# Kernel tuning notes

Measured on AMD Instinct MI355X. Metric: run time of the kernel, lower is better.

Reference implementation:

```python
import jax, jax.numpy as jnp
import numpy as np
import math

A, R, E, H = 4, 2, 12, 24  # msg_angular, msg_radial, embed_dim, hidden_dim
N = A * R
B, L = 131072, 15

def _ring_adj(n):
    adj = np.zeros((n, n), np.float32)
    if n == 1:
        adj[0, 0] = 1.0
    else:
        for i in range(n):
            adj[i, (i - 1) % n] = 1.0
            adj[i, (i + 1) % n] = 1.0
    return jnp.asarray(adj)

ANG_ADJ = _ring_adj(A)
RAD_ADJ = _ring_adj(R)

def setup_inputs():
    key = jax.random.key(0)
    ks = jax.random.split(key, 16)
    p = lambda k, s: jax.random.normal(k, s, jnp.float32) * 0.1
    return {
        "x": jax.random.normal(ks[0], (B, L, 4), jnp.float32),
        "enc_w1": p(ks[1], (4, H)), "enc_b1": p(ks[2], (H,)),
        "enc_w2": p(ks[3], (H, H)), "enc_b2": p(ks[4], (H,)),
        "enc_w3": p(ks[5], (H, 3)), "enc_b3": p(ks[6], (3,)),
        "node_w1": p(ks[7], (E, H)), "node_b1": p(ks[8], (H,)),
        "node_w2": p(ks[9], (H, E)), "node_b2": p(ks[10], (E,)),
        "angular_logit": jnp.zeros((A,), jnp.float32),
        "radial_logit": jnp.zeros((R,), jnp.float32),
        "read_w1": p(ks[11], (E * N, H)), "read_b1": p(ks[12], (H,)),
        "read_w2": p(ks[13], (H, 4)), "read_b2": p(ks[14], (4,)),
    }

def _norm_adj(logit, adj):
    a = jax.nn.softmax(logit)[None, :] * adj
    return a / jnp.maximum(a.sum(1, keepdims=True), 1e-6)

def _forward(x, enc_w1, enc_b1, enc_w2, enc_b2, enc_w3, enc_b3,
             node_w1, node_b1, node_w2, node_b2,
             angular_logit, radial_logit,
             read_w1, read_b1, read_w2, read_b2):
    b = x.shape[0]
    # encoder: original loops over all timesteps but only uses the last z
    zt = jnp.tanh(x[:, -1, :] @ enc_w1 + enc_b1)
    zt = jnp.tanh(zt @ enc_w2 + enc_b2)
    z = zt @ enc_w3 + enc_b3                       # [B, 3]
    r = jax.nn.sigmoid(z[:, 0]) * (R - 1)          # R_idx in [0, R-1]
    p = (z[:, 1] + math.pi) / (2 * math.pi) * A    # phi_idx (can be <0 or >A)
    # torch code calls .item(), detaching indices/weights from autograd
    r = jax.lax.stop_gradient(r)
    p = jax.lax.stop_gradient(p)
    r0 = jnp.trunc(r)   # int() truncates toward zero
    p0 = jnp.trunc(p)
    dr = (r - r0)[:, None]
    dp = (p - p0)[:, None]
    dro = jnp.array([0.0, 0.0, 1.0, 1.0], jnp.float32)   # 4 bilinear corners
    dpo = jnp.array([0.0, 1.0, 0.0, 1.0], jnp.float32)
    wr = jnp.where(dro == 0, 1.0 - dr, dr)               # [B, 4]
    wp = jnp.where(dpo == 0, 1.0 - dp, dp)
    w = wr * wp                                          # [B, 4]
    r_i = jnp.minimum(r0.astype(jnp.int32)[:, None] + dro.astype(jnp.int32), R - 1)
    p_i = jnp.mod(p0.astype(jnp.int32)[:, None] + dpo.astype(jnp.int32), A)
    mask = (w > 0).astype(x.dtype)[:, :, None]           # 'if weight > 0' skip
    # node_embed = pad(concat([z, weight]), E); z entries are NOT weight-scaled
    vec = jnp.concatenate([
        jnp.broadcast_to(z[:, None, :], (b, 4, 3)),
        w[:, :, None],
        jnp.zeros((b, 4, E - 4), x.dtype)], axis=-1) * mask   # [B, 4, E]
    grid = jnp.zeros((b, R, A, E), x.dtype).at[
        jnp.arange(b)[:, None], r_i, p_i].add(vec)            # scatter-add
    h = grid.reshape(b, N, E)
    ang = _norm_adj(angular_logit, ANG_ADJ)  # [A, A]
    rad = _norm_adj(radial_logit, RAD_ADJ)   # [R, R]
    # faithful to the torch .view() layout mixing (r,a,e)
    h_ang = jnp.einsum('ij,bjk->bik', ang, h.reshape(b, A, R * E)).reshape(b, N, E)
    h_rad = jnp.einsum('ij,bjk->bik', rad, h.reshape(b, R, A * E)).reshape(b, N, E)
    h = h + h_ang + h_rad
    h = jnp.tanh(h @ node_w1 + node_b1) @ node_w2 + node_b2   # node_net
    out = jnp.tanh(h.reshape(b, -1) @ read_w1 + read_b1) @ read_w2 + read_b2
    return out  # [B, 4]

def reference(x, enc_w1, enc_b1, enc_w2, enc_b2, enc_w3, enc_b3,
              node_w1, node_b1, node_w2, node_b2,
              angular_logit, radial_logit,
              read_w1, read_b1, read_w2, read_b2):
    return _forward(x, enc_w1, enc_b1, enc_w2, enc_b2, enc_w3, enc_b3,
                    node_w1, node_b1, node_w2, node_b2,
                    angular_logit, radial_logit,
                    read_w1, read_b1, read_w2, read_b2)
```

## Files before the change

### kernel.cpp

```cpp
#include <hip/hip_runtime.h>
#include <math.h>


#define PI_F 3.14159265358979323846f

__device__ __forceinline__ float fast_tanh(float v) {
    float e = __expf(2.0f * v);
    return 1.0f - 2.0f * __builtin_amdgcn_rcpf(e + 1.0f);
}

__device__ __forceinline__ float quad_sum(float x) {
    x += __int_as_float(__builtin_amdgcn_update_dpp(
             0, __float_as_int(x), 0xB1, 0xF, 0xF, true));
    x += __int_as_float(__builtin_amdgcn_update_dpp(
             0, __float_as_int(x), 0x4E, 0xF, 0xF, true));
    return x;
}

#define K1_LDS 800

extern "C" __global__ void __launch_bounds__(256, 2)
topo_k1(const float* __restrict__ x,
        const float* __restrict__ ew1, const float* __restrict__ eb1,
        const float* __restrict__ ew2, const float* __restrict__ eb2,
        const float* __restrict__ ew3, const float* __restrict__ eb3,
        const float* __restrict__ alog, const float* __restrict__ rlog,
        float* __restrict__ ws, int B)
{
    __shared__ float wf[K1_LDS];
    const float4* wq = reinterpret_cast<const float4*>(wf);
    {
        const int tt = threadIdx.x;
        for (int i = tt; i < 96;  i += 256) wf[i]       = ew1[i];
        for (int i = tt; i < 24;  i += 256) wf[96 + i]  = eb1[i];
        for (int i = tt; i < 576; i += 256) wf[120 + i] = ew2[i];
        for (int i = tt; i < 24;  i += 256) wf[696 + i] = eb2[i];
        for (int i = tt; i < 72;  i += 256) wf[720 + (i % 3) * 24 + (i / 3)] = ew3[i];
        for (int i = tt; i < 3;   i += 256) wf[792 + i] = eb3[i];
    }
    __syncthreads();

    const int b = blockIdx.x * blockDim.x + threadIdx.x;
    if (b >= B) return;

    float ang[4][4];
    {
        float m = fmaxf(fmaxf(alog[0], alog[1]), fmaxf(alog[2], alog[3]));
        float e0 = __expf(alog[0] - m), e1 = __expf(alog[1] - m);
        float e2 = __expf(alog[2] - m), e3 = __expf(alog[3] - m);
        float s = e0 + e1 + e2 + e3;
        float sm[4] = { e0 / s, e1 / s, e2 / s, e3 / s };
        #pragma unroll
        for (int i = 0; i < 4; ++i) {
            const int jn = (i + 3) & 3, jp = (i + 1) & 3;
            float inv = 1.0f / fmaxf(sm[jn] + sm[jp], 1e-6f);
            #pragma unroll
            for (int j = 0; j < 4; ++j) {
                float adj = (j == jn || j == jp) ? 1.0f : 0.0f;
                ang[i][j] = sm[j] * adj * inv;
            }
        }
    }
    float rad[2][2];
    {
        float m = fmaxf(rlog[0], rlog[1]);
        float f0 = __expf(rlog[0] - m), f1 = __expf(rlog[1] - m);
        float fs = f0 + f1;
        float sm0 = f0 / fs, sm1 = f1 / fs;
        rad[0][0] = 0.0f; rad[0][1] = sm1 / fmaxf(sm1, 1e-6f);
        rad[1][1] = 0.0f; rad[1][0] = sm0 / fmaxf(sm0, 1e-6f);
    }

    const float4 xv = *reinterpret_cast<const float4*>(x + (size_t)b * 60 + 56);

    float zt[24];
    #pragma unroll
    for (int c = 0; c < 6; ++c) {
        float4 b4 = wq[24 + c];
        float4 w0 = wq[c],      w1 = wq[6 + c];
        float4 w2 = wq[12 + c], w3 = wq[18 + c];
        zt[c*4+0] = fast_tanh(b4.x + xv.x*w0.x + xv.y*w1.x + xv.z*w2.x + xv.w*w3.x);
        zt[c*4+1] = fast_tanh(b4.y + xv.x*w0.y + xv.y*w1.y + xv.z*w2.y + xv.w*w3.y);
        zt[c*4+2] = fast_tanh(b4.z + xv.x*w0.z + xv.y*w1.z + xv.z*w2.z + xv.w*w3.z);
        zt[c*4+3] = fast_tanh(b4.w + xv.x*w0.w + xv.y*w1.w + xv.z*w2.w + xv.w*w3.w);
    }

    float a2[24];
    #pragma unroll
    for (int c = 0; c < 6; ++c) {
        float4 b4 = wq[174 + c];
        a2[c*4+0] = b4.x; a2[c*4+1] = b4.y; a2[c*4+2] = b4.z; a2[c*4+3] = b4.w;
    }
    #pragma unroll
    for (int k = 0; k < 24; ++k) {
        const float zk = zt[k];
        #pragma unroll
        for (int c = 0; c < 6; ++c) {
            float4 wv = wq[30 + k * 6 + c];
            a2[c*4+0] += zk * wv.x; a2[c*4+1] += zk * wv.y;
            a2[c*4+2] += zk * wv.z; a2[c*4+3] += zk * wv.w;
        }
    }
    float zt2[24];
    #pragma unroll
    for (int j = 0; j < 24; ++j) zt2[j] = fast_tanh(a2[j]);

    float z0 = wf[792], z1 = wf[793], z2 = wf[794];
    #pragma unroll
    for (int c = 0; c < 6; ++c) {
        float4 v0 = wq[180 + c], v1 = wq[186 + c], v2 = wq[192 + c];
        z0 += zt2[c*4+0]*v0.x + zt2[c*4+1]*v0.y + zt2[c*4+2]*v0.z + zt2[c*4+3]*v0.w;
        z1 += zt2[c*4+0]*v1.x + zt2[c*4+1]*v1.y + zt2[c*4+2]*v1.z + zt2[c*4+3]*v1.w;
        z2 += zt2[c*4+0]*v2.x + zt2[c*4+1]*v2.y + zt2[c*4+2]*v2.z + zt2[c*4+3]*v2.w;
    }

    const float r = 1.0f / (1.0f + __expf(-z0));
    const float p = (z1 + PI_F) / (2.0f * PI_F) * 4.0f;
    const float r0f = truncf(r), p0f = truncf(p);
    const float dr = r - r0f, dp = p - p0f;
    const int r0i = (int)r0f, p0i = (int)p0f;

    const float w0c = (1.0f - dr) * (1.0f - dp);
    const float w1c = (1.0f - dr) * dp;
    const float w2c = dr * (1.0f - dp);
    const float w3c = dr * dp;

    const int ri0 = min(r0i, 1);
    const int ri2 = min(r0i + 1, 1);
    const int pi0 = p0i & 3;
    const int pi1 = (p0i + 1) & 3;

    const int c0 = ri0 * 4 + pi0, c1 = ri0 * 4 + pi1;
    const int c2 = ri2 * 4 + pi0, c3 = ri2 * 4 + pi1;

    float cnt[8], wsum[8];
    #pragma unroll
    for (int n = 0; n < 8; ++n) {
        float cm = 0.0f, cw = 0.0f;
        if (c0 == n && w0c > 0.0f) { cm += 1.0f; cw += w0c; }
        if (c1 == n && w1c > 0.0f) { cm += 1.0f; cw += w1c; }
        if (c2 == n && w2c > 0.0f) { cm += 1.0f; cw += w2c; }
        if (c3 == n && w3c > 0.0f) { cm += 1.0f; cw += w3c; }
        cnt[n] = cm; wsum[n] = cw;
    }
    float mc[8], mw[8];
    #pragma unroll
    for (int n = 0; n < 8; ++n) {
        float ac = cnt[n], aw = wsum[n];
        #pragma unroll
        for (int j = 0; j < 4; ++j) {
            const float g = ang[n >> 1][j];
            ac += g * cnt[2 * j + (n & 1)];
            aw += g * wsum[2 * j + (n & 1)];
        }
        #pragma unroll
        for (int j = 0; j < 2; ++j) {
            const float g = rad[n >> 2][j];
            ac += g * cnt[4 * j + (n & 3)];
            aw += g * wsum[4 * j + (n & 3)];
        }
        mc[n] = ac; mw[n] = aw;
    }

    float* wp = ws + (size_t)b * 20;
    float4 v0; v0.x = z0;    v0.y = z1;    v0.z = z2;    v0.w = 0.0f;
    float4 v1; v1.x = mc[0]; v1.y = mc[1]; v1.z = mc[2]; v1.w = mc[3];
    float4 v2; v2.x = mc[4]; v2.y = mc[5]; v2.z = mc[6]; v2.w = mc[7];
    float4 v3; v3.x = mw[0]; v3.y = mw[1]; v3.z = mw[2]; v3.w = mw[3];
    float4 v4; v4.x = mw[4]; v4.y = mw[5]; v4.z = mw[6]; v4.w = mw[7];
    reinterpret_cast<float4*>(wp)[0] = v0;
    reinterpret_cast<float4*>(wp)[1] = v1;
    reinterpret_cast<float4*>(wp)[2] = v2;
    reinterpret_cast<float4*>(wp)[3] = v3;
    reinterpret_cast<float4*>(wp)[4] = v4;
}

#define K2_LDS 2912

extern "C" __global__ void __launch_bounds__(256, 6)
topo_k2(const float* __restrict__ ws,
        const float* __restrict__ nw1, const float* __restrict__ nb1,
        const float* __restrict__ nw2, const float* __restrict__ nb2,
        const float* __restrict__ rw1, const float* __restrict__ rb1,
        const float* __restrict__ rw2, const float* __restrict__ rb2,
        float* __restrict__ out, int B)
{
    __shared__ float wf[K2_LDS];
    const float4* wq = reinterpret_cast<const float4*>(wf);

    {
        const int tt = threadIdx.x;
        for (int i = tt; i < 96;   i += 256) wf[i]        = nw1[i];
        for (int i = tt; i < 24;   i += 256) wf[96 + i]   = nb1[i];
        for (int i = tt; i < 288;  i += 256) wf[120 + i]  = nw2[i];
        for (int i = tt; i < 12;   i += 256) wf[408 + i]  = nb2[i];
        for (int i = tt; i < 2304; i += 256) {
            const int cell = i / 288, rem = i - cell * 288;
            wf[420 + cell * 296 + rem] = rw1[i];
        }
        for (int i = tt; i < 24;   i += 256) wf[2788 + i] = rb1[i];
        for (int i = tt; i < 96;   i += 256) wf[2812 + i] = rw2[i];
        for (int i = tt; i < 4;    i += 256) wf[2908 + i] = rb2[i];
    }
    __syncthreads();

    const int tid  = blockIdx.x * blockDim.x + threadIdx.x;
    const int lane = tid & 3;
    const int b    = tid >> 2;
    if (b >= B) return;

    const float* wp = ws + (size_t)b * 20;
    const float4 zv = *reinterpret_cast<const float4*>(wp);
    const float2 mc2 = *reinterpret_cast<const float2*>(wp + 4 + 2 * lane);
    const float2 mw2 = *reinterpret_cast<const float2*>(wp + 12 + 2 * lane);
    const float z0 = zv.x, z1 = zv.y, z2 = zv.z;

    float t[24];
    #pragma unroll
    for (int j = 0; j < 24; ++j) t[j] = 0.0f;

    #pragma unroll
    for (int cc = 0; cc < 2; ++cc) {
        const float mc_ = cc ? mc2.y : mc2.x;
        const float mw_ = cc ? mw2.y : mw2.x;
        const float f0 = mc_ * z0, f1 = mc_ * z1, f2 = mc_ * z2;

        float ho[12];
        {
            float4 bA = wq[102], bB = wq[103], bC = wq[104];
            ho[0] = bA.x; ho[1]  = bA.y; ho[2]  = bA.z; ho[3]  = bA.w;
            ho[4] = bB.x; ho[5]  = bB.y; ho[6]  = bB.z; ho[7]  = bB.w;
            ho[8] = bC.x; ho[9]  = bC.y; ho[10] = bC.z; ho[11] = bC.w;
        }
        #pragma unroll
        for (int c = 0; c < 6; ++c) {
            float4 b1 = wq[24 + c];
            float4 u0 = wq[c],      u1 = wq[6 + c];
            float4 u2 = wq[12 + c], u3 = wq[18 + c];
            float h[4];
            h[0] = fast_tanh(b1.x + f0*u0.x + f1*u1.x + f2*u2.x + mw_*u3.x);
            h[1] = fast_tanh(b1.y + f0*u0.y + f1*u1.y + f2*u2.y + mw_*u3.y);
            h[2] = fast_tanh(b1.z + f0*u0.z + f1*u1.z + f2*u2.z + mw_*u3.z);
            h[3] = fast_tanh(b1.w + f0*u0.w + f1*u1.w + f2*u2.w + mw_*u3.w);
            #pragma unroll
            for (int jj = 0; jj < 4; ++jj) {
                const int j = c * 4 + jj;
                const float hj = h[jj];
                float4 n0 = wq[30 + j * 3], n1 = wq[31 + j * 3], n2 = wq[32 + j * 3];
                ho[0] += hj*n0.x; ho[1]  += hj*n0.y; ho[2]  += hj*n0.z; ho[3]  += hj*n0.w;
                ho[4] += hj*n1.x; ho[5]  += hj*n1.y; ho[6]  += hj*n1.z; ho[7]  += hj*n1.w;
                ho[8] += hj*n2.x; ho[9]  += hj*n2.y; ho[10] += hj*n2.z; ho[11] += hj*n2.w;
            }
        }
        const int cellbase = 420 + (2 * lane + cc) * 296;
        #pragma unroll
        for (int d = 0; d < 12; ++d) {
            const float hd = ho[d];
            const int qb = (cellbase >> 2) + d * 6;
            #pragma unroll
            for (int c = 0; c < 6; ++c) {
                float4 rv = wq[qb + c];
                t[c*4+0] += hd * rv.x; t[c*4+1] += hd * rv.y;
                t[c*4+2] += hd * rv.z; t[c*4+3] += hd * rv.w;
            }
        }
        __builtin_amdgcn_sched_barrier(0);
    }

    #pragma unroll
    for (int j = 0; j < 24; ++j) t[j] = quad_sum(t[j]) + wf[2788 + j];

    float4 ob = wq[727];
    float o0 = ob.x, o1 = ob.y, o2 = ob.z, o3 = ob.w;
    #pragma unroll
    for (int j = 0; j < 24; ++j) {
        const float tv = fast_tanh(t[j]);
        float4 rv = wq[703 + j];
        o0 += tv * rv.x; o1 += tv * rv.y; o2 += tv * rv.z; o3 += tv * rv.w;
    }
    if (lane == 0) {
        float4 ov; ov.x = o0; ov.y = o1; ov.z = o2; ov.w = o3;
        *reinterpret_cast<float4*>(out + (size_t)b * 4) = ov;
    }
}

extern "C" __global__ void __launch_bounds__(256, 2)
topo_fused(const float* __restrict__ x,
           const float* __restrict__ ew1, const float* __restrict__ eb1,
           const float* __restrict__ ew2, const float* __restrict__ eb2,
           const float* __restrict__ ew3, const float* __restrict__ eb3,
           const float* __restrict__ nw1, const float* __restrict__ nb1,
           const float* __restrict__ nw2, const float* __restrict__ nb2,
           const float* __restrict__ alog, const float* __restrict__ rlog,
           const float* __restrict__ rw1, const float* __restrict__ rb1,
           const float* __restrict__ rw2, const float* __restrict__ rb2,
           float* __restrict__ out, int B)
{
    const int b = blockIdx.x * blockDim.x + threadIdx.x;
    if (b >= B) return;

    float ang[4][4];
    {
        float m = fmaxf(fmaxf(alog[0], alog[1]), fmaxf(alog[2], alog[3]));
        float e0 = __expf(alog[0] - m), e1 = __expf(alog[1] - m);
        float e2 = __expf(alog[2] - m), e3 = __expf(alog[3] - m);
        float s = e0 + e1 + e2 + e3;
        float sm[4] = { e0 / s, e1 / s, e2 / s, e3 / s };
        #pragma unroll
        for (int i = 0; i < 4; ++i) {
            const int jn = (i + 3) & 3, jp = (i + 1) & 3;
            float inv = 1.0f / fmaxf(sm[jn] + sm[jp], 1e-6f);
            #pragma unroll
            for (int j = 0; j < 4; ++j) {
                float adj = (j == jn || j == jp) ? 1.0f : 0.0f;
                ang[i][j] = sm[j] * adj * inv;
            }
        }
    }
    float rad[2][2];
    {
        float m = fmaxf(rlog[0], rlog[1]);
        float f0 = __expf(rlog[0] - m), f1 = __expf(rlog[1] - m);
        float fs = f0 + f1;
        float sm0 = f0 / fs, sm1 = f1 / fs;
        rad[0][0] = 0.0f; rad[0][1] = sm1 / fmaxf(sm1, 1e-6f);
        rad[1][1] = 0.0f; rad[1][0] = sm0 / fmaxf(sm0, 1e-6f);
    }

    const float4 xv = *reinterpret_cast<const float4*>(x + (size_t)b * 60 + 56);
    float zt[24];
    #pragma unroll
    for (int j = 0; j < 24; ++j) {
        float a = eb1[j];
        a += xv.x * ew1[j];
        a += xv.y * ew1[24 + j];
        a += xv.z * ew1[48 + j];
        a += xv.w * ew1[72 + j];
        zt[j] = fast_tanh(a);
    }
    float z0 = eb3[0], z1 = eb3[1], z2 = eb3[2];
    #pragma unroll
    for (int j = 0; j < 24; ++j) {
        float a = eb2[j];
        #pragma unroll
        for (int k = 0; k < 24; ++k) a += zt[k] * ew2[k * 24 + j];
        const float z2t = fast_tanh(a);
        z0 += z2t * ew3[j * 3 + 0];
        z1 += z2t * ew3[j * 3 + 1];
        z2 += z2t * ew3[j * 3 + 2];
    }

    const float r = 1.0f / (1.0f + __expf(-z0));
    const float p = (z1 + PI_F) / (2.0f * PI_F) * 4.0f;
    const float r0f = truncf(r), p0f = truncf(p);
    const float dr = r - r0f, dp = p - p0f;
    const int r0i = (int)r0f, p0i = (int)p0f;
    const float w0c = (1.0f - dr) * (1.0f - dp);
    const float w1c = (1.0f - dr) * dp;
    const float w2c = dr * (1.0f - dp);
    const float w3c = dr * dp;
    const int ri0 = min(r0i, 1);
    const int ri2 = min(r0i + 1, 1);
    const int pi0 = p0i & 3;
    const int pi1 = (p0i + 1) & 3;
    const int c0 = ri0 * 4 + pi0, c1 = ri0 * 4 + pi1;
    const int c2 = ri2 * 4 + pi0, c3 = ri2 * 4 + pi1;

    float cnt[8], wsum[8];
    #pragma unroll
    for (int n = 0; n < 8; ++n) {
        float cm = 0.0f, cw = 0.0f;
        if (c0 == n && w0c > 0.0f) { cm += 1.0f; cw += w0c; }
        if (c1 == n && w1c > 0.0f) { cm += 1.0f; cw += w1c; }
        if (c2 == n && w2c > 0.0f) { cm += 1.0f; cw += w2c; }
        if (c3 == n && w3c > 0.0f) { cm += 1.0f; cw += w3c; }
        cnt[n] = cm; wsum[n] = cw;
    }
    float mc[8], mw[8];
    #pragma unroll
    for (int n = 0; n < 8; ++n) {
        float ac = cnt[n], aw = wsum[n];
        #pragma unroll
        for (int j = 0; j < 4; ++j) {
            const float g = ang[n >> 1][j];
            ac += g * cnt[2 * j + (n & 1)];
            aw += g * wsum[2 * j + (n & 1)];
        }
        #pragma unroll
        for (int j = 0; j < 2; ++j) {
            const float g = rad[n >> 2][j];
            ac += g * cnt[4 * j + (n & 3)];
            aw += g * wsum[4 * j + (n & 3)];
        }
        mc[n] = ac; mw[n] = aw;
    }

    float t[24];
    #pragma unroll
    for (int j = 0; j < 24; ++j) t[j] = rb1[j];
    #pragma unroll
    for (int n = 0; n < 8; ++n) {
        const float f0 = mc[n] * z0, f1 = mc[n] * z1, f2 = mc[n] * z2;
        float ho[12];
        #pragma unroll
        for (int d = 0; d < 12; ++d) ho[d] = nb2[d];
        #pragma unroll
        for (int j = 0; j < 24; ++j) {
            const float hj = fast_tanh(nb1[j] + f0 * nw1[j] + f1 * nw1[24 + j]
                                       + f2 * nw1[48 + j] + mw[n] * nw1[72 + j]);
            #pragma unroll
            for (int d = 0; d < 12; ++d) ho[d] += hj * nw2[j * 12 + d];
        }
        #pragma unroll
        for (int d = 0; d < 12; ++d) {
            const int rbase = (n * 12 + d) * 24;
            #pragma unroll
            for (int j2 = 0; j2 < 24; ++j2) t[j2] += ho[d] * rw1[rbase + j2];
        }
    }

    float o0 = rb2[0], o1 = rb2[1], o2 = rb2[2], o3 = rb2[3];
    #pragma unroll
    for (int j = 0; j < 24; ++j) {
        const float tt = fast_tanh(t[j]);
        o0 += tt * rw2[j * 4 + 0];
        o1 += tt * rw2[j * 4 + 1];
        o2 += tt * rw2[j * 4 + 2];
        o3 += tt * rw2[j * 4 + 3];
    }
    float4 ov; ov.x = o0; ov.y = o1; ov.z = o2; ov.w = o3;
    *reinterpret_cast<float4*>(out + (size_t)b * 4) = ov;
}

extern "C" void kernel_launch(void* const* d_in, const int* in_sizes, int n_in,
                              void* d_out, int out_size, void* d_ws, size_t ws_size,
                              hipStream_t stream) {
    const float* x    = (const float*)d_in[0];
    const float* ew1  = (const float*)d_in[1];
    const float* eb1  = (const float*)d_in[2];
    const float* ew2  = (const float*)d_in[3];
    const float* eb2  = (const float*)d_in[4];
    const float* ew3  = (const float*)d_in[5];
    const float* eb3  = (const float*)d_in[6];
    const float* nw1  = (const float*)d_in[7];
    const float* nb1  = (const float*)d_in[8];
    const float* nw2  = (const float*)d_in[9];
    const float* nb2  = (const float*)d_in[10];
    const float* alog = (const float*)d_in[11];
    const float* rlog = (const float*)d_in[12];
    const float* rw1  = (const float*)d_in[13];
    const float* rb1  = (const float*)d_in[14];
    const float* rw2  = (const float*)d_in[15];
    const float* rb2  = (const float*)d_in[16];
    float* out = (float*)d_out;

    const int B = in_sizes[0] / 60;
    const size_t ws_needed = (size_t)B * 20 * sizeof(float);

    if (ws_size >= ws_needed) {
        float* ws = (float*)d_ws;
        const int g1 = (B + 255) / 256;
        topo_k1<<<g1, 256, 0, stream>>>(x, ew1, eb1, ew2, eb2, ew3, eb3,
                                        alog, rlog, ws, B);
        const long long tot2 = (long long)B * 4;
        const int g2 = (int)((tot2 + 255) / 256);
        topo_k2<<<g2, 256, 0, stream>>>(ws, nw1, nb1, nw2, nb2,
                                        rw1, rb1, rw2, rb2, out, B);
    } else {
        const int g = (B + 255) / 256;
        topo_fused<<<g, 256, 0, stream>>>(
            x, ew1, eb1, ew2, eb2, ew3, eb3, nw1, nb1, nw2, nb2,
            alog, rlog, rw1, rb1, rw2, rb2, out, B);
    }
}
```

Measured before the change: 51.61 us.

## Split encoder hidden layer across thread pairs and fuse both cells in node MLP

The first kernel now uses two threads per sample. Each thread computes half of the second encoder layer and its partial contribution to the three outputs, and the halves are combined with a DPP lane swap. The second kernel processes both grid cells of a lane together, sharing the z-dependent products and interleaving the readout accumulation for the two cells. The goal is more parallelism and less per-thread serial work, at the cost of duplicated first-layer tanh work, twice as many threads in the first kernel, and higher register pressure in the second kernel.

```diff
diff --git a/kernel.cpp b/kernel.cpp
--- a/kernel.cpp
+++ b/kernel.cpp
@@ -7,6 +7,12 @@
 __device__ __forceinline__ float fast_tanh(float v) {
     float e = __expf(2.0f * v);
     return 1.0f - 2.0f * __builtin_amdgcn_rcpf(e + 1.0f);
+}
+
+__device__ __forceinline__ float pair_sum(float x) {
+    x += __int_as_float(__builtin_amdgcn_update_dpp(
+             0, __float_as_int(x), 0xB1, 0xF, 0xF, true));
+    return x;
 }
 
 __device__ __forceinline__ float quad_sum(float x) {
@@ -40,8 +46,57 @@
     }
     __syncthreads();
 
-    const int b = blockIdx.x * blockDim.x + threadIdx.x;
+    const int tid = blockIdx.x * blockDim.x + threadIdx.x;
+    const int h   = tid & 1;
+    const int b   = tid >> 1;
     if (b >= B) return;
+
+    const float4 xv = *reinterpret_cast<const float4*>(x + (size_t)b * 60 + 56);
+
+    float zt[24];
+    #pragma unroll
+    for (int c = 0; c < 6; ++c) {
+        float4 b4 = wq[24 + c];
+        float4 w0 = wq[c],      w1 = wq[6 + c];
+        float4 w2 = wq[12 + c], w3 = wq[18 + c];
+        zt[c*4+0] = fast_tanh(b4.x + xv.x*w0.x + xv.y*w1.x + xv.z*w2.x + xv.w*w3.x);
+        zt[c*4+1] = fast_tanh(b4.y + xv.x*w0.y + xv.y*w1.y + xv.z*w2.y + xv.w*w3.y);
+        zt[c*4+2] = fast_tanh(b4.z + xv.x*w0.z + xv.y*w1.z + xv.z*w2.z + xv.w*w3.z);
+        zt[c*4+3] = fast_tanh(b4.w + xv.x*w0.w + xv.y*w1.w + xv.z*w2.w + xv.w*w3.w);
+    }
+
+    const int h3 = 3 * h;
+    float a2h[12];
+    #pragma unroll
+    for (int c = 0; c < 3; ++c) {
+        float4 b4 = wq[174 + h3 + c];
+        a2h[c*4+0] = b4.x; a2h[c*4+1] = b4.y; a2h[c*4+2] = b4.z; a2h[c*4+3] = b4.w;
+    }
+    #pragma unroll
+    for (int k = 0; k < 24; ++k) {
+        const float zk = zt[k];
+        #pragma unroll
+        for (int c = 0; c < 3; ++c) {
+            float4 wv = wq[30 + 6 * k + h3 + c];
+            a2h[c*4+0] += zk * wv.x; a2h[c*4+1] += zk * wv.y;
+            a2h[c*4+2] += zk * wv.z; a2h[c*4+3] += zk * wv.w;
+        }
+    }
+    float zt2h[12];
+    #pragma unroll
+    for (int j = 0; j < 12; ++j) zt2h[j] = fast_tanh(a2h[j]);
+
+    float z0p = 0.0f, z1p = 0.0f, z2p = 0.0f;
+    #pragma unroll
+    for (int c = 0; c < 3; ++c) {
+        float4 v0 = wq[180 + h3 + c], v1 = wq[186 + h3 + c], v2 = wq[192 + h3 + c];
+        z0p += zt2h[c*4+0]*v0.x + zt2h[c*4+1]*v0.y + zt2h[c*4+2]*v0.z + zt2h[c*4+3]*v0.w;
+        z1p += zt2h[c*4+0]*v1.x + zt2h[c*4+1]*v1.y + zt2h[c*4+2]*v1.z + zt2h[c*4+3]*v1.w;
+        z2p += zt2h[c*4+0]*v2.x + zt2h[c*4+1]*v2.y + zt2h[c*4+2]*v2.z + zt2h[c*4+3]*v2.w;
+    }
+    const float z0 = pair_sum(z0p) + wf[792];
+    const float z1 = pair_sum(z1p) + wf[793];
+    const float z2 = pair_sum(z2p) + wf[794];
 
     float ang[4][4];
     {
@@ -71,49 +126,6 @@
         rad[1][1] = 0.0f; rad[1][0] = sm0 / fmaxf(sm0, 1e-6f);
     }
 
-    const float4 xv = *reinterpret_cast<const float4*>(x + (size_t)b * 60 + 56);
-
-    float zt[24];
-    #pragma unroll
-    for (int c = 0; c < 6; ++c) {
-        float4 b4 = wq[24 + c];
-        float4 w0 = wq[c],      w1 = wq[6 + c];
-        float4 w2 = wq[12 + c], w3 = wq[18 + c];
-        zt[c*4+0] = fast_tanh(b4.x + xv.x*w0.x + xv.y*w1.x + xv.z*w2.x + xv.w*w3.x);
-        zt[c*4+1] = fast_tanh(b4.y + xv.x*w0.y + xv.y*w1.y + xv.z*w2.y + xv.w*w3.y);
-        zt[c*4+2] = fast_tanh(b4.z + xv.x*w0.z + xv.y*w1.z + xv.z*w2.z + xv.w*w3.z);
-        zt[c*4+3] = fast_tanh(b4.w + xv.x*w0.w + xv.y*w1.w + xv.z*w2.w + xv.w*w3.w);
-    }
-
-    float a2[24];
-    #pragma unroll
-    for (int c = 0; c < 6; ++c) {
-        float4 b4 = wq[174 + c];
-        a2[c*4+0] = b4.x; a2[c*4+1] = b4.y; a2[c*4+2] = b4.z; a2[c*4+3] = b4.w;
-    }
-    #pragma unroll
-    for (int k = 0; k < 24; ++k) {
-        const float zk = zt[k];
-        #pragma unroll
-        for (int c = 0; c < 6; ++c) {
-            float4 wv = wq[30 + k * 6 + c];
-            a2[c*4+0] += zk * wv.x; a2[c*4+1] += zk * wv.y;
-            a2[c*4+2] += zk * wv.z; a2[c*4+3] += zk * wv.w;
-        }
-    }
-    float zt2[24];
-    #pragma unroll
-    for (int j = 0; j < 24; ++j) zt2[j] = fast_tanh(a2[j]);
-
-    float z0 = wf[792], z1 = wf[793], z2 = wf[794];
-    #pragma unroll
-    for (int c = 0; c < 6; ++c) {
-        float4 v0 = wq[180 + c], v1 = wq[186 + c], v2 = wq[192 + c];
-        z0 += zt2[c*4+0]*v0.x + zt2[c*4+1]*v0.y + zt2[c*4+2]*v0.z + zt2[c*4+3]*v0.w;
-        z1 += zt2[c*4+0]*v1.x + zt2[c*4+1]*v1.y + zt2[c*4+2]*v1.z + zt2[c*4+3]*v1.w;
-        z2 += zt2[c*4+0]*v2.x + zt2[c*4+1]*v2.y + zt2[c*4+2]*v2.z + zt2[c*4+3]*v2.w;
-    }
-
     const float r = 1.0f / (1.0f + __expf(-z0));
     const float p = (z1 + PI_F) / (2.0f * PI_F) * 4.0f;
     const float r0f = truncf(r), p0f = truncf(p);
@@ -162,17 +174,19 @@
         mc[n] = ac; mw[n] = aw;
     }
 
-    float* wp = ws + (size_t)b * 20;
-    float4 v0; v0.x = z0;    v0.y = z1;    v0.z = z2;    v0.w = 0.0f;
-    float4 v1; v1.x = mc[0]; v1.y = mc[1]; v1.z = mc[2]; v1.w = mc[3];
-    float4 v2; v2.x = mc[4]; v2.y = mc[5]; v2.z = mc[6]; v2.w = mc[7];
-    float4 v3; v3.x = mw[0]; v3.y = mw[1]; v3.z = mw[2]; v3.w = mw[3];
-    float4 v4; v4.x = mw[4]; v4.y = mw[5]; v4.z = mw[6]; v4.w = mw[7];
-    reinterpret_cast<float4*>(wp)[0] = v0;
-    reinterpret_cast<float4*>(wp)[1] = v1;
-    reinterpret_cast<float4*>(wp)[2] = v2;
-    reinterpret_cast<float4*>(wp)[3] = v3;
-    reinterpret_cast<float4*>(wp)[4] = v4;
+    if (h == 0) {
+        float* wp = ws + (size_t)b * 20;
+        float4 v0; v0.x = z0;    v0.y = z1;    v0.z = z2;    v0.w = 0.0f;
+        float4 v1; v1.x = mc[0]; v1.y = mc[1]; v1.z = mc[2]; v1.w = mc[3];
+        float4 v2; v2.x = mc[4]; v2.y = mc[5]; v2.z = mc[6]; v2.w = mc[7];
+        float4 v3; v3.x = mw[0]; v3.y = mw[1]; v3.z = mw[2]; v3.w = mw[3];
+        float4 v4; v4.x = mw[4]; v4.y = mw[5]; v4.z = mw[6]; v4.w = mw[7];
+        reinterpret_cast<float4*>(wp)[0] = v0;
+        reinterpret_cast<float4*>(wp)[1] = v1;
+        reinterpret_cast<float4*>(wp)[2] = v2;
+        reinterpret_cast<float4*>(wp)[3] = v3;
+        reinterpret_cast<float4*>(wp)[4] = v4;
+    }
 }
 
 #define K2_LDS 2912
@@ -214,57 +228,82 @@
     const float2 mc2 = *reinterpret_cast<const float2*>(wp + 4 + 2 * lane);
     const float2 mw2 = *reinterpret_cast<const float2*>(wp + 12 + 2 * lane);
     const float z0 = zv.x, z1 = zv.y, z2 = zv.z;
+    const float mcA = mc2.x, mcB = mc2.y, mwA = mw2.x, mwB = mw2.y;
+
+    float hoA[12], hoB[12];
+    {
+        float4 bA = wq[102], bB = wq[103], bC = wq[104];
+        hoA[0] = bA.x; hoA[1]  = bA.y; hoA[2]  = bA.z; hoA[3]  = bA.w;
+        hoA[4] = bB.x; hoA[5]  = bB.y; hoA[6]  = bB.z; hoA[7]  = bB.w;
+        hoA[8] = bC.x; hoA[9]  = bC.y; hoA[10] = bC.z; hoA[11] = bC.w;
+        #pragma unroll
+        for (int d = 0; d < 12; ++d) hoB[d] = hoA[d];
+    }
+    #pragma unroll
+    for (int c = 0; c < 6; ++c) {
+        float4 b1 = wq[24 + c];
+        float4 u0 = wq[c],      u1 = wq[6 + c];
+        float4 u2 = wq[12 + c], u3 = wq[18 + c];
+        const float q0 = z0*u0.x + z1*u1.x + z2*u2.x;
+        const float q1 = z0*u0.y + z1*u1.y + z2*u2.y;
+        const float q2 = z0*u0.z + z1*u1.z + z2*u2.z;
+        const float q3 = z0*u0.w + z1*u1.w + z2*u2.w;
+        float hA[4], hB[4];
+        hA[0] = fast_tanh(b1.x + mcA*q0 + mwA*u3.x);
+        hA[1] = fast_tanh(b1.y + mcA*q1 + mwA*u3.y);
+        hA[2] = fast_tanh(b1.z + mcA*q2 + mwA*u3.z);
+        hA[3] = fast_tanh(b1.w + mcA*q3 + mwA*u3.w);
+        hB[0] = fast_tanh(b1.x + mcB*q0 + mwB*u3.x);
+        hB[1] = fast_tanh(b1.y + mcB*q1 + mwB*u3.y);
+        hB[2] = fast_tanh(b1.z + mcB*q2 + mwB*u3.z);
+        hB[3] = fast_tanh(b1.w + mcB*q3 + mwB*u3.w);
+        #pragma unroll
+        for (int jj = 0; jj < 4; ++jj) {
+            const int j = c * 4 + jj;
+            const float ha = hA[jj], hb = hB[jj];
+            float4 n0 = wq[30 + j * 3], n1 = wq[31 + j * 3], n2 = wq[32 + j * 3];
+            hoA[0] += ha*n0.x; hoA[1]  += ha*n0.y; hoA[2]  += ha*n0.z; hoA[3]  += ha*n0.w;
+            hoA[4] += ha*n1.x; hoA[5]  += ha*n1.y; hoA[6]  += ha*n1.z; hoA[7]  += ha*n1.w;
+            hoA[8] += ha*n2.x; hoA[9]  += ha*n2.y; hoA[10] += ha*n2.z; hoA[11] += ha*n2.w;
+            hoB[0] += hb*n0.x; hoB[1]  += hb*n0.y; hoB[2]  += hb*n0.z; hoB[3]  += hb*n0.w;
+            hoB[4] += hb*n1.x; hoB[5]  += hb*n1.y; hoB[6]  += hb*n1.z; hoB[7]  += hb*n1.w;
+            hoB[8] += hb*n2.x; hoB[9]  += hb*n2.y; hoB[10] += hb*n2.z; hoB[11] += hb*n2.w;
+        }
+        __builtin_amdgcn_sched_barrier(0);
+    }
 
     float t[24];
     #pragma unroll
     for (int j = 0; j < 24; ++j) t[j] = 0.0f;
 
-    #pragma unroll
-    for (int cc = 0; cc < 2; ++cc) {
-        const float mc_ = cc ? mc2.y : mc2.x;
-        const float mw_ = cc ? mw2.y : mw2.x;
-        const float f0 = mc_ * z0, f1 = mc_ * z1, f2 = mc_ * z2;
-
-        float ho[12];
-        {
-            float4 bA = wq[102], bB = wq[103], bC = wq[104];
-            ho[0] = bA.x; ho[1]  = bA.y; ho[2]  = bA.z; ho[3]  = bA.w;
-            ho[4] = bB.x; ho[5]  = bB.y; ho[6]  = bB.z; ho[7]  = bB.w;
-            ho[8] = bC.x; ho[9]  = bC.y; ho[10] = bC.z; ho[11] = bC.w;
-        }
+    const int qbA = 105 + (2 * lane) * 74;
+    const int qbB = qbA + 74;
+    #pragma unroll
+    for (int d = 0; d < 6; ++d) {
+        const float ha = hoA[d], hb = hoB[d];
         #pragma unroll
         for (int c = 0; c < 6; ++c) {
-            float4 b1 = wq[24 + c];
-            float4 u0 = wq[c],      u1 = wq[6 + c];
-            float4 u2 = wq[12 + c], u3 = wq[18 + c];
-            float h[4];
-            h[0] = fast_tanh(b1.x + f0*u0.x + f1*u1.x + f2*u2.x + mw_*u3.x);
-            h[1] = fast_tanh(b1.y + f0*u0.y + f1*u1.y + f2*u2.y + mw_*u3.y);
-            h[2] = fast_tanh(b1.z + f0*u0.z + f1*u1.z + f2*u2.z + mw_*u3.z);
-            h[3] = fast_tanh(b1.w + f0*u0.w + f1*u1.w + f2*u2.w + mw_*u3.w);
-            #pragma unroll
-            for (int jj = 0; jj < 4; ++jj) {
-                const int j = c * 4 + jj;
-                const float hj = h[jj];
-                float4 n0 = wq[30 + j * 3], n1 = wq[31 + j * 3], n2 = wq[32 + j * 3];
-                ho[0] += hj*n0.x; ho[1]  += hj*n0.y; ho[2]  += hj*n0.z; ho[3]  += hj*n0.w;
-                ho[4] += hj*n1.x; ho[5]  += hj*n1.y; ho[6]  += hj*n1.z; ho[7]  += hj*n1.w;
-                ho[8] += hj*n2.x; ho[9]  += hj*n2.y; ho[10] += hj*n2.z; ho[11] += hj*n2.w;
-            }
-        }
-        const int cellbase = 420 + (2 * lane + cc) * 296;
-        #pragma unroll
-        for (int d = 0; d < 12; ++d) {
-            const float hd = ho[d];
-            const int qb = (cellbase >> 2) + d * 6;
-            #pragma unroll
-            for (int c = 0; c < 6; ++c) {
-                float4 rv = wq[qb + c];
-                t[c*4+0] += hd * rv.x; t[c*4+1] += hd * rv.y;
-                t[c*4+2] += hd * rv.z; t[c*4+3] += hd * rv.w;
-            }
-        }
-        __builtin_amdgcn_sched_barrier(0);
+            float4 rvA = wq[qbA + d * 6 + c];
+            float4 rvB = wq[qbB + d * 6 + c];
+            t[c*4+0] += ha * rvA.x + hb * rvB.x;
+            t[c*4+1] += ha * rvA.y + hb * rvB.y;
+            t[c*4+2] += ha * rvA.z + hb * rvB.z;
+            t[c*4+3] += ha * rvA.w + hb * rvB.w;
+        }
+    }
+    __builtin_amdgcn_sched_barrier(0);
+    #pragma unroll
+    for (int d = 6; d < 12; ++d) {
+        const float ha = hoA[d], hb = hoB[d];
+        #pragma unroll
+        for (int c = 0; c < 6; ++c) {
+            float4 rvA = wq[qbA + d * 6 + c];
+            float4 rvB = wq[qbB + d * 6 + c];
+            t[c*4+0] += ha * rvA.x + hb * rvB.x;
+            t[c*4+1] += ha * rvA.y + hb * rvB.y;
+            t[c*4+2] += ha * rvA.z + hb * rvB.z;
+            t[c*4+3] += ha * rvA.w + hb * rvB.w;
+        }
     }
 
     #pragma unroll
@@ -459,7 +498,8 @@
 
     if (ws_size >= ws_needed) {
         float* ws = (float*)d_ws;
-        const int g1 = (B + 255) / 256;
+        const long long tot1 = (long long)B * 2;
+        const int g1 = (int)((tot1 + 255) / 256);
         topo_k1<<<g1, 256, 0, stream>>>(x, ew1, eb1, ew2, eb2, ew3, eb3,
                                         alog, rlog, ws, B);
         const long long tot2 = (long long)B * 4;
```

Result: no change. 52.04 us (+0.8%).

## Fold node_w2 into readout weights and precompute the fused matrix in extra blocks

Applied to the files above, without the earlier changes.

Extra blocks appended to the first kernel precompute M = node_w2 · read_w1 per cell, plus a combined bias, and write them to the workspace. The second kernel then skips the 12-wide node output layer and accumulates each 24-wide hidden activation directly into the readout. It also exploits the rank structure of the node input (mc·z plus mw) to compute the first node layer more cheaply. Encoder weights are repacked so layer one's tanh is interleaved with layer two in a non-unrolled loop. The trade-offs are a larger LDS footprint in the second kernel, which may lower occupancy, and weight preprocessing that now runs on every call.

```diff
diff --git a/kernel.cpp b/kernel.cpp
--- a/kernel.cpp
+++ b/kernel.cpp
@@ -17,7 +17,7 @@
     return x;
 }
 
-#define K1_LDS 800
+#define K1_LDS 880
 
 extern "C" __global__ void __launch_bounds__(256, 2)
 topo_k1(const float* __restrict__ x,
@@ -25,23 +25,89 @@
         const float* __restrict__ ew2, const float* __restrict__ eb2,
         const float* __restrict__ ew3, const float* __restrict__ eb3,
         const float* __restrict__ alog, const float* __restrict__ rlog,
+        const float* __restrict__ nw2, const float* __restrict__ nb2,
+        const float* __restrict__ rw1, const float* __restrict__ rb1,
         float* __restrict__ ws, int B)
 {
+    const int nb1b = (B + 255) >> 8;
+
+    if ((int)blockIdx.x >= nb1b) {
+        const int gid = ((int)blockIdx.x - nb1b) * 256 + (int)threadIdx.x;
+        float* M = ws + (size_t)B * 20;
+        if (gid < 4608) {
+            const int cell = gid / 576, rem = gid - cell * 576;
+            const int j = rem / 24, j2 = rem - j * 24;
+            float s = 0.0f;
+            #pragma unroll
+            for (int d = 0; d < 12; ++d)
+                s += nw2[j * 12 + d] * rw1[(cell * 12 + d) * 24 + j2];
+            M[gid] = s;
+        } else if (gid < 4632) {
+            const int j2 = gid - 4608;
+            float s = rb1[j2];
+            for (int i = 0; i < 96; ++i)
+                s += nb2[i % 12] * rw1[i * 24 + j2];
+            M[4608 + j2] = s;
+        }
+        return;
+    }
+
     __shared__ float wf[K1_LDS];
     const float4* wq = reinterpret_cast<const float4*>(wf);
     {
         const int tt = threadIdx.x;
-        for (int i = tt; i < 96;  i += 256) wf[i]       = ew1[i];
-        for (int i = tt; i < 24;  i += 256) wf[96 + i]  = eb1[i];
-        for (int i = tt; i < 576; i += 256) wf[120 + i] = ew2[i];
-        for (int i = tt; i < 24;  i += 256) wf[696 + i] = eb2[i];
-        for (int i = tt; i < 72;  i += 256) wf[720 + (i % 3) * 24 + (i / 3)] = ew3[i];
-        for (int i = tt; i < 3;   i += 256) wf[792 + i] = eb3[i];
+        for (int i = tt; i < 24; i += 256) {
+            wf[i * 8 + 0] = ew1[i];
+            wf[i * 8 + 1] = ew1[24 + i];
+            wf[i * 8 + 2] = ew1[48 + i];
+            wf[i * 8 + 3] = ew1[72 + i];
+            wf[i * 8 + 4] = eb1[i];
+        }
+        for (int i = tt; i < 576; i += 256) wf[192 + i] = ew2[i];
+        for (int i = tt; i < 24;  i += 256) wf[768 + i] = eb2[i];
+        for (int i = tt; i < 72;  i += 256) wf[792 + (i % 3) * 24 + (i / 3)] = ew3[i];
+        for (int i = tt; i < 3;   i += 256) wf[864 + i] = eb3[i];
     }
     __syncthreads();
 
     const int b = blockIdx.x * blockDim.x + threadIdx.x;
     if (b >= B) return;
+
+    const float4 xv = *reinterpret_cast<const float4*>(x + (size_t)b * 60 + 56);
+
+    float a2[24];
+    #pragma unroll
+    for (int c = 0; c < 6; ++c) {
+        float4 b4 = wq[192 / 4 + c];
+        a2[c*4+0] = b4.x; a2[c*4+1] = b4.y; a2[c*4+2] = b4.z; a2[c*4+3] = b4.w;
+    }
+    #pragma unroll 1
+    for (int k = 0; k < 24; ++k) {
+        float4 p  = wq[2 * k];
+        float4 p2 = wq[2 * k + 1];
+        const float zk = fast_tanh(p2.x + xv.x*p.x + xv.y*p.y + xv.z*p.z + xv.w*p.w);
+        const int rr = 48 + k * 6;
+        float4 r0 = wq[rr+0], r1 = wq[rr+1], r2 = wq[rr+2];
+        float4 r3 = wq[rr+3], r4 = wq[rr+4], r5 = wq[rr+5];
+        a2[0]+=zk*r0.x; a2[1]+=zk*r0.y; a2[2]+=zk*r0.z; a2[3]+=zk*r0.w;
+        a2[4]+=zk*r1.x; a2[5]+=zk*r1.y; a2[6]+=zk*r1.z; a2[7]+=zk*r1.w;
+        a2[8]+=zk*r2.x; a2[9]+=zk*r2.y; a2[10]+=zk*r2.z; a2[11]+=zk*r2.w;
+        a2[12]+=zk*r3.x; a2[13]+=zk*r3.y; a2[14]+=zk*r3.z; a2[15]+=zk*r3.w;
+        a2[16]+=zk*r4.x; a2[17]+=zk*r4.y; a2[18]+=zk*r4.z; a2[19]+=zk*r4.w;
+        a2[20]+=zk*r5.x; a2[21]+=zk*r5.y; a2[22]+=zk*r5.z; a2[23]+=zk*r5.w;
+    }
+    float zt2[24];
+    #pragma unroll
+    for (int j = 0; j < 24; ++j) zt2[j] = fast_tanh(a2[j]);
+
+    float z0 = wf[864], z1 = wf[865], z2 = wf[866];
+    #pragma unroll
+    for (int c = 0; c < 6; ++c) {
+        float4 v0 = wq[198 + c], v1 = wq[204 + c], v2 = wq[210 + c];
+        z0 += zt2[c*4+0]*v0.x + zt2[c*4+1]*v0.y + zt2[c*4+2]*v0.z + zt2[c*4+3]*v0.w;
+        z1 += zt2[c*4+0]*v1.x + zt2[c*4+1]*v1.y + zt2[c*4+2]*v1.z + zt2[c*4+3]*v1.w;
+        z2 += zt2[c*4+0]*v2.x + zt2[c*4+1]*v2.y + zt2[c*4+2]*v2.z + zt2[c*4+3]*v2.w;
+    }
 
     float ang[4][4];
     {
@@ -69,49 +135,6 @@
         float sm0 = f0 / fs, sm1 = f1 / fs;
         rad[0][0] = 0.0f; rad[0][1] = sm1 / fmaxf(sm1, 1e-6f);
         rad[1][1] = 0.0f; rad[1][0] = sm0 / fmaxf(sm0, 1e-6f);
-    }
-
-    const float4 xv = *reinterpret_cast<const float4*>(x + (size_t)b * 60 + 56);
-
-    float zt[24];
-    #pragma unroll
-    for (int c = 0; c < 6; ++c) {
-        float4 b4 = wq[24 + c];
-        float4 w0 = wq[c],      w1 = wq[6 + c];
-        float4 w2 = wq[12 + c], w3 = wq[18 + c];
-        zt[c*4+0] = fast_tanh(b4.x + xv.x*w0.x + xv.y*w1.x + xv.z*w2.x + xv.w*w3.x);
-        zt[c*4+1] = fast_tanh(b4.y + xv.x*w0.y + xv.y*w1.y + xv.z*w2.y + xv.w*w3.y);
-        zt[c*4+2] = fast_tanh(b4.z + xv.x*w0.z + xv.y*w1.z + xv.z*w2.z + xv.w*w3.z);
-        zt[c*4+3] = fast_tanh(b4.w + xv.x*w0.w + xv.y*w1.w + xv.z*w2.w + xv.w*w3.w);
-    }
-
-    float a2[24];
-    #pragma unroll
-    for (int c = 0; c < 6; ++c) {
-        float4 b4 = wq[174 + c];
-        a2[c*4+0] = b4.x; a2[c*4+1] = b4.y; a2[c*4+2] = b4.z; a2[c*4+3] = b4.w;
-    }
-    #pragma unroll
-    for (int k = 0; k < 24; ++k) {
-        const float zk = zt[k];
-        #pragma unroll
-        for (int c = 0; c < 6; ++c) {
-            float4 wv = wq[30 + k * 6 + c];
-            a2[c*4+0] += zk * wv.x; a2[c*4+1] += zk * wv.y;
-            a2[c*4+2] += zk * wv.z; a2[c*4+3] += zk * wv.w;
-        }
-    }
-    float zt2[24];
-    #pragma unroll
-    for (int j = 0; j < 24; ++j) zt2[j] = fast_tanh(a2[j]);
-
-    float z0 = wf[792], z1 = wf[793], z2 = wf[794];
-    #pragma unroll
-    for (int c = 0; c < 6; ++c) {
-        float4 v0 = wq[180 + c], v1 = wq[186 + c], v2 = wq[192 + c];
-        z0 += zt2[c*4+0]*v0.x + zt2[c*4+1]*v0.y + zt2[c*4+2]*v0.z + zt2[c*4+3]*v0.w;
-        z1 += zt2[c*4+0]*v1.x + zt2[c*4+1]*v1.y + zt2[c*4+2]*v1.z + zt2[c*4+3]*v1.w;
-        z2 += zt2[c*4+0]*v2.x + zt2[c*4+1]*v2.y + zt2[c*4+2]*v2.z + zt2[c*4+3]*v2.w;
     }
 
     const float r = 1.0f / (1.0f + __expf(-z0));
@@ -175,32 +198,33 @@
     reinterpret_cast<float4*>(wp)[4] = v4;
 }
 
-#define K2_LDS 2912
-
-extern "C" __global__ void __launch_bounds__(256, 6)
+#define K2_LDS 4956
+
+extern "C" __global__ void __launch_bounds__(256)
 topo_k2(const float* __restrict__ ws,
         const float* __restrict__ nw1, const float* __restrict__ nb1,
-        const float* __restrict__ nw2, const float* __restrict__ nb2,
-        const float* __restrict__ rw1, const float* __restrict__ rb1,
         const float* __restrict__ rw2, const float* __restrict__ rb2,
         float* __restrict__ out, int B)
 {
     __shared__ float wf[K2_LDS];
     const float4* wq = reinterpret_cast<const float4*>(wf);
-
     {
         const int tt = threadIdx.x;
-        for (int i = tt; i < 96;   i += 256) wf[i]        = nw1[i];
-        for (int i = tt; i < 24;   i += 256) wf[96 + i]   = nb1[i];
-        for (int i = tt; i < 288;  i += 256) wf[120 + i]  = nw2[i];
-        for (int i = tt; i < 12;   i += 256) wf[408 + i]  = nb2[i];
-        for (int i = tt; i < 2304; i += 256) {
-            const int cell = i / 288, rem = i - cell * 288;
-            wf[420 + cell * 296 + rem] = rw1[i];
-        }
-        for (int i = tt; i < 24;   i += 256) wf[2788 + i] = rb1[i];
-        for (int i = tt; i < 96;   i += 256) wf[2812 + i] = rw2[i];
-        for (int i = tt; i < 4;    i += 256) wf[2908 + i] = rb2[i];
+        const float* Msrc = ws + (size_t)B * 20;
+        for (int i = tt; i < 4608; i += 256) {
+            const int cell = i / 576, rem = i - cell * 576;
+            wf[192 + cell * 580 + rem] = Msrc[i];
+        }
+        for (int i = tt; i < 24; i += 256) wf[4832 + i] = Msrc[4608 + i];
+        for (int i = tt; i < 24; i += 256) {
+            wf[i * 8 + 0] = nw1[i];
+            wf[i * 8 + 1] = nw1[24 + i];
+            wf[i * 8 + 2] = nw1[48 + i];
+            wf[i * 8 + 3] = nw1[72 + i];
+            wf[i * 8 + 4] = nb1[i];
+        }
+        for (int i = tt; i < 96; i += 256) wf[4856 + i] = rw2[i];
+        for (int i = tt; i < 4;  i += 256) wf[4952 + i] = rb2[i];
     }
     __syncthreads();
 
@@ -214,68 +238,50 @@
     const float2 mc2 = *reinterpret_cast<const float2*>(wp + 4 + 2 * lane);
     const float2 mw2 = *reinterpret_cast<const float2*>(wp + 12 + 2 * lane);
     const float z0 = zv.x, z1 = zv.y, z2 = zv.z;
+    const float mcA = mc2.x, mcB = mc2.y, mwA = mw2.x, mwB = mw2.y;
+
+    const int mAq = 48 + (2 * lane) * 145;
+    const int mBq = mAq + 145;
 
     float t[24];
     #pragma unroll
     for (int j = 0; j < 24; ++j) t[j] = 0.0f;
 
-    #pragma unroll
-    for (int cc = 0; cc < 2; ++cc) {
-        const float mc_ = cc ? mc2.y : mc2.x;
-        const float mw_ = cc ? mw2.y : mw2.x;
-        const float f0 = mc_ * z0, f1 = mc_ * z1, f2 = mc_ * z2;
-
-        float ho[12];
-        {
-            float4 bA = wq[102], bB = wq[103], bC = wq[104];
-            ho[0] = bA.x; ho[1]  = bA.y; ho[2]  = bA.z; ho[3]  = bA.w;
-            ho[4] = bB.x; ho[5]  = bB.y; ho[6]  = bB.z; ho[7]  = bB.w;
-            ho[8] = bC.x; ho[9]  = bC.y; ho[10] = bC.z; ho[11] = bC.w;
-        }
-        #pragma unroll
-        for (int c = 0; c < 6; ++c) {
-            float4 b1 = wq[24 + c];
-            float4 u0 = wq[c],      u1 = wq[6 + c];
-            float4 u2 = wq[12 + c], u3 = wq[18 + c];
-            float h[4];
-            h[0] = fast_tanh(b1.x + f0*u0.x + f1*u1.x + f2*u2.x + mw_*u3.x);
-            h[1] = fast_tanh(b1.y + f0*u0.y + f1*u1.y + f2*u2.y + mw_*u3.y);
-            h[2] = fast_tanh(b1.z + f0*u0.z + f1*u1.z + f2*u2.z + mw_*u3.z);
-            h[3] = fast_tanh(b1.w + f0*u0.w + f1*u1.w + f2*u2.w + mw_*u3.w);
-            #pragma unroll
-            for (int jj = 0; jj < 4; ++jj) {
-                const int j = c * 4 + jj;
-                const float hj = h[jj];
-                float4 n0 = wq[30 + j * 3], n1 = wq[31 + j * 3], n2 = wq[32 + j * 3];
-                ho[0] += hj*n0.x; ho[1]  += hj*n0.y; ho[2]  += hj*n0.z; ho[3]  += hj*n0.w;
-                ho[4] += hj*n1.x; ho[5]  += hj*n1.y; ho[6]  += hj*n1.z; ho[7]  += hj*n1.w;
-                ho[8] += hj*n2.x; ho[9]  += hj*n2.y; ho[10] += hj*n2.z; ho[11] += hj*n2.w;
-            }
-        }
-        const int cellbase = 420 + (2 * lane + cc) * 296;
-        #pragma unroll
-        for (int d = 0; d < 12; ++d) {
-            const float hd = ho[d];
-            const int qb = (cellbase >> 2) + d * 6;
-            #pragma unroll
-            for (int c = 0; c < 6; ++c) {
-                float4 rv = wq[qb + c];
-                t[c*4+0] += hd * rv.x; t[c*4+1] += hd * rv.y;
-                t[c*4+2] += hd * rv.z; t[c*4+3] += hd * rv.w;
-            }
-        }
-        __builtin_amdgcn_sched_barrier(0);
-    }
-
-    #pragma unroll
-    for (int j = 0; j < 24; ++j) t[j] = quad_sum(t[j]) + wf[2788 + j];
-
-    float4 ob = wq[727];
+    #pragma unroll 1
+    for (int j = 0; j < 24; ++j) {
+        float4 pk  = wq[2 * j];
+        float4 pk2 = wq[2 * j + 1];
+        const float q  = z0 * pk.x + z1 * pk.y + z2 * pk.z;
+        const float hA = fast_tanh(pk2.x + mcA * q + mwA * pk.w);
+        const float hB = fast_tanh(pk2.x + mcB * q + mwB * pk.w);
+        const int ra = mAq + j * 6, rb = mBq + j * 6;
+        float4 a0 = wq[ra+0], a1 = wq[ra+1], a2v = wq[ra+2];
+        float4 a3 = wq[ra+3], a4 = wq[ra+4], a5  = wq[ra+5];
+        float4 b0 = wq[rb+0], b1 = wq[rb+1], b2v = wq[rb+2];
+        float4 b3 = wq[rb+3], b4 = wq[rb+4], b5  = wq[rb+5];
+        t[0]  += hA*a0.x  + hB*b0.x;  t[1]  += hA*a0.y  + hB*b0.y;
+        t[2]  += hA*a0.z  + hB*b0.z;  t[3]  += hA*a0.w  + hB*b0.w;
+        t[4]  += hA*a1.x  + hB*b1.x;  t[5]  += hA*a1.y  + hB*b1.y;
+        t[6]  += hA*a1.z  + hB*b1.z;  t[7]  += hA*a1.w  + hB*b1.w;
+        t[8]  += hA*a2v.x + hB*b2v.x; t[9]  += hA*a2v.y + hB*b2v.y;
+        t[10] += hA*a2v.z + hB*b2v.z; t[11] += hA*a2v.w + hB*b2v.w;
+        t[12] += hA*a3.x  + hB*b3.x;  t[13] += hA*a3.y  + hB*b3.y;
+        t[14] += hA*a3.z  + hB*b3.z;  t[15] += hA*a3.w  + hB*b3.w;
+        t[16] += hA*a4.x  + hB*b4.x;  t[17] += hA*a4.y  + hB*b4.y;
+        t[18] += hA*a4.z  + hB*b4.z;  t[19] += hA*a4.w  + hB*b4.w;
+        t[20] += hA*a5.x  + hB*b5.x;  t[21] += hA*a5.y  + hB*b5.y;
+        t[22] += hA*a5.z  + hB*b5.z;  t[23] += hA*a5.w  + hB*b5.w;
+    }
+
+    #pragma unroll
+    for (int j = 0; j < 24; ++j) t[j] = quad_sum(t[j]) + wf[4832 + j];
+
+    float4 ob = wq[1238];
     float o0 = ob.x, o1 = ob.y, o2 = ob.z, o3 = ob.w;
     #pragma unroll
     for (int j = 0; j < 24; ++j) {
         const float tv = fast_tanh(t[j]);
-        float4 rv = wq[703 + j];
+        float4 rv = wq[1214 + j];
         o0 += tv * rv.x; o1 += tv * rv.y; o2 += tv * rv.z; o3 += tv * rv.w;
     }
     if (lane == 0) {
@@ -455,17 +461,17 @@
     float* out = (float*)d_out;
 
     const int B = in_sizes[0] / 60;
-    const size_t ws_needed = (size_t)B * 20 * sizeof(float);
+    const size_t ws_needed = ((size_t)B * 20 + 4632) * sizeof(float);
 
     if (ws_size >= ws_needed) {
         float* ws = (float*)d_ws;
-        const int g1 = (B + 255) / 256;
+        const int nb1b = (B + 255) / 256;
+        const int g1 = nb1b + 19;
         topo_k1<<<g1, 256, 0, stream>>>(x, ew1, eb1, ew2, eb2, ew3, eb3,
-                                        alog, rlog, ws, B);
+                                        alog, rlog, nw2, nb2, rw1, rb1, ws, B);
         const long long tot2 = (long long)B * 4;
         const int g2 = (int)((tot2 + 255) / 256);
-        topo_k2<<<g2, 256, 0, stream>>>(ws, nw1, nb1, nw2, nb2,
-                                        rw1, rb1, rw2, rb2, out, B);
+        topo_k2<<<g2, 256, 0, stream>>>(ws, nw1, nb1, rw2, rb2, out, B);
     } else {
         const int g = (B + 255) / 256;
         topo_fused<<<g, 256, 0, stream>>>(
```

New measurement: 54.04 us. 1.05x slower.
